# Optimization experiments

Hardware: AMD Instinct MI355X
Metric: run time of the kernel (lower is better)

## Reference

```python
import jax, jax.numpy as jnp
import numpy as np

# Dimensions: batch B, time dims P,Q, grids N, hidden nhid
B, P, Q, N, NHID = 4, 6, 4, 512, 32
WD = 4 * NHID          # wd1 = wd2 = nhid*4 = 128
AD = 2 * WD            # ad = 2*nhid*4 = 256
ALPHA = 0.2            # LeakyReLU negative slope


def setup_inputs() -> dict:
    key = jax.random.key(0)
    k1, k2, k3, k4 = jax.random.split(key, 4)
    demand = jax.random.uniform(k1, (B, P, Q, N, N), dtype=jnp.float32)
    st_feat = jax.random.normal(k2, (B, P, Q, N, WD), dtype=jnp.float32)
    # xavier_uniform with gain=1.414
    lim_W = 1.414 * np.sqrt(6.0 / (WD + WD))
    W = jax.random.uniform(k3, (WD, WD), minval=-lim_W, maxval=lim_W, dtype=jnp.float32)
    lim_a = 1.414 * np.sqrt(6.0 / (AD + 1))
    a = jax.random.uniform(k4, (AD, 1), minval=-lim_a, maxval=lim_a, dtype=jnp.float32)
    return {"demand": demand, "st_feat": st_feat, "W": W, "a": a}


def reference(demand, st_feat, W, a):
    # h = st_feat @ W : [B,P,Q,N,WD]
    h = st_feat @ W
    # GAT algebraic split: a^T [h_i || h_j] = a1.h_i + a2.h_j
    # (same math as torch repeat/cat/matmul, without the O(N^2*AD) intermediate)
    a1 = a[:WD, 0]
    a2 = a[WD:, 0]
    s1 = h @ a1  # [B,P,Q,N] -- score contribution from node i (repeated rows)
    s2 = h @ a2  # [B,P,Q,N] -- score contribution from node j (tiled rows)
    e = jax.nn.leaky_relu(s1[..., :, None] + s2[..., None, :], negative_slope=ALPHA)
    attention = jax.nn.softmax(e, axis=-1)  # softmax over j (dim=4)
    # dropout omitted: eval-mode deterministic reference
    od_matrix = jax.nn.leaky_relu(demand * attention, negative_slope=ALPHA)
    return od_matrix
```

## Files before the change

### kernel.cpp

```cpp
#include <hip/hip_runtime.h>

#define NB 4
#define NP 6
#define NQ 4
#define NN 512
#define NWD 128
#define NBPQ (NB * NP * NQ)
#define NROWS (NBPQ * NN)
#define ALPHA 0.2f

__device__ __forceinline__ float lrelu(float x) {
    return x > 0.f ? x : ALPHA * x;
}

__global__ void wa_kernel(const float* __restrict__ W, const float* __restrict__ a,
                          float* __restrict__ wa) {
    int t = threadIdx.x;
    int k = t & (NWD - 1);
    int half = t >> 7;
    const float* av = a + half * NWD;
    const float* wr = W + (long)k * NWD;
    float s = 0.f;
    #pragma unroll 8
    for (int d = 0; d < NWD; ++d) s += wr[d] * av[d];
    wa[half * NWD + k] = s;
}

__global__ __launch_bounds__(256) void s_kernel(const float* __restrict__ st,
                                                const float* __restrict__ wa,
                                                float* __restrict__ s1,
                                                float* __restrict__ s2) {
    int wid = threadIdx.x >> 6;
    int lane = threadIdx.x & 63;
    long g = (long)blockIdx.x * 4 + wid;
    const float2 f  = *reinterpret_cast<const float2*>(st + g * NWD + lane * 2);
    const float2 w1 = *reinterpret_cast<const float2*>(wa + lane * 2);
    const float2 w2 = *reinterpret_cast<const float2*>(wa + NWD + lane * 2);
    float p1 = f.x * w1.x + f.y * w1.y;
    float p2 = f.x * w2.x + f.y * w2.y;
    #pragma unroll
    for (int off = 32; off > 0; off >>= 1) {
        p1 += __shfl_xor(p1, off);
        p2 += __shfl_xor(p2, off);
    }
    if (lane == 0) { s1[g] = p1; s2[g] = p2; }
}

__global__ __launch_bounds__(256) void main_kernel(const float* __restrict__ demand,
                                                   const float* __restrict__ s1,
                                                   const float* __restrict__ s2,
                                                   float* __restrict__ out) {
    int wid = threadIdx.x >> 6;
    int lane = threadIdx.x & 63;
    long g = (long)blockIdx.x * 4 + wid;
    long slice = g >> 9;
    float s1i = s1[g];
    const float* s2s = s2 + slice * NN;

    const int c0 = lane * 4;
    const int c1 = 256 + lane * 4;
    const float4 sa = *reinterpret_cast<const float4*>(s2s + c0);
    const float4 sb = *reinterpret_cast<const float4*>(s2s + c1);

    float e[8];
    e[0] = lrelu(s1i + sa.x); e[1] = lrelu(s1i + sa.y);
    e[2] = lrelu(s1i + sa.z); e[3] = lrelu(s1i + sa.w);
    e[4] = lrelu(s1i + sb.x); e[5] = lrelu(s1i + sb.y);
    e[6] = lrelu(s1i + sb.z); e[7] = lrelu(s1i + sb.w);

    float m = e[0];
    #pragma unroll
    for (int k = 1; k < 8; ++k) m = fmaxf(m, e[k]);
    #pragma unroll
    for (int off = 32; off > 0; off >>= 1) m = fmaxf(m, __shfl_xor(m, off));

    float p[8];
    float sum = 0.f;
    #pragma unroll
    for (int k = 0; k < 8; ++k) { p[k] = expf(e[k] - m); sum += p[k]; }
    #pragma unroll
    for (int off = 32; off > 0; off >>= 1) sum += __shfl_xor(sum, off);
    const float inv = 1.f / sum;

    const float* drow = demand + g * NN;
    const float4 d0 = *reinterpret_cast<const float4*>(drow + c0);
    const float4 d1 = *reinterpret_cast<const float4*>(drow + c1);

    float4 o0, o1;
    o0.x = lrelu(d0.x * p[0] * inv); o0.y = lrelu(d0.y * p[1] * inv);
    o0.z = lrelu(d0.z * p[2] * inv); o0.w = lrelu(d0.w * p[3] * inv);
    o1.x = lrelu(d1.x * p[4] * inv); o1.y = lrelu(d1.y * p[5] * inv);
    o1.z = lrelu(d1.z * p[6] * inv); o1.w = lrelu(d1.w * p[7] * inv);

    float* orow = out + g * NN;
    *reinterpret_cast<float4*>(orow + c0) = o0;
    *reinterpret_cast<float4*>(orow + c1) = o1;
}

extern "C" void kernel_launch(void* const* d_in, const int* in_sizes, int n_in,
                              void* d_out, int out_size, void* d_ws, size_t ws_size,
                              hipStream_t stream) {
    const float* demand  = (const float*)d_in[0];
    const float* st_feat = (const float*)d_in[1];
    const float* W       = (const float*)d_in[2];
    const float* a       = (const float*)d_in[3];
    float* out = (float*)d_out;

    float* wa = (float*)d_ws;
    float* s1 = wa + 2 * NWD;
    float* s2 = s1 + NROWS;

    wa_kernel<<<1, 256, 0, stream>>>(W, a, wa);
    s_kernel<<<NROWS / 4, 256, 0, stream>>>(st_feat, wa, s1, s2);
    main_kernel<<<NROWS / 4, 256, 0, stream>>>(demand, s1, s2, out);
}
```

Measured before the change: 50.22 us.

## Fuse W·a projection into score kernel and process more rows per block

Drops the single-block wa kernel. Each block of the score kernel now recomputes W·a1 and W·a2 into shared memory, then handles 64 rows with float4 loads, two rows per wave iteration and a 32-lane reduction. This removes one launch and the serial dependency on a one-block kernel, and cuts the score kernel's grid size. The cost is that every block redundantly reads all of W, 64 KB. The softmax also switches to the fast __expf intrinsic, which is slightly less accurate.

Result: slower. 54.07 us (+7.7%).

```diff
diff --git a/kernel.cpp b/kernel.cpp
--- a/kernel.cpp
+++ b/kernel.cpp
@@ -5,45 +5,62 @@
 #define NQ 4
 #define NN 512
 #define NWD 128
-#define NBPQ (NB * NP * NQ)
-#define NROWS (NBPQ * NN)
+#define NROWS (NB * NP * NQ * NN)
 #define ALPHA 0.2f
 
 __device__ __forceinline__ float lrelu(float x) {
     return x > 0.f ? x : ALPHA * x;
 }
 
-__global__ void wa_kernel(const float* __restrict__ W, const float* __restrict__ a,
-                          float* __restrict__ wa) {
-    int t = threadIdx.x;
-    int k = t & (NWD - 1);
-    int half = t >> 7;
-    const float* av = a + half * NWD;
-    const float* wr = W + (long)k * NWD;
-    float s = 0.f;
-    #pragma unroll 8
-    for (int d = 0; d < NWD; ++d) s += wr[d] * av[d];
-    wa[half * NWD + k] = s;
-}
+__global__ __launch_bounds__(256) void s_fused_kernel(const float* __restrict__ st,
+                                                      const float* __restrict__ W,
+                                                      const float* __restrict__ a,
+                                                      float* __restrict__ s1,
+                                                      float* __restrict__ s2) {
+    __shared__ float wa1[NWD];
+    __shared__ float wa2[NWD];
 
-__global__ __launch_bounds__(256) void s_kernel(const float* __restrict__ st,
-                                                const float* __restrict__ wa,
-                                                float* __restrict__ s1,
-                                                float* __restrict__ s2) {
-    int wid = threadIdx.x >> 6;
-    int lane = threadIdx.x & 63;
-    long g = (long)blockIdx.x * 4 + wid;
-    const float2 f  = *reinterpret_cast<const float2*>(st + g * NWD + lane * 2);
-    const float2 w1 = *reinterpret_cast<const float2*>(wa + lane * 2);
-    const float2 w2 = *reinterpret_cast<const float2*>(wa + NWD + lane * 2);
-    float p1 = f.x * w1.x + f.y * w1.y;
-    float p2 = f.x * w2.x + f.y * w2.y;
+    const int t = threadIdx.x;
+    const int wid = t >> 6;
+    const int lane = t & 63;
+
+    {
+        const int k = t & (NWD - 1);
+        const float* av = a + (t >> 7) * NWD;
+        const float* wr = W + (long)k * NWD;
+        float s = 0.f;
+        #pragma unroll
+        for (int d = 0; d < NWD; d += 4) {
+            const float4 wv  = *reinterpret_cast<const float4*>(wr + d);
+            const float4 avv = *reinterpret_cast<const float4*>(av + d);
+            s += wv.x * avv.x + wv.y * avv.y + wv.z * avv.z + wv.w * avv.w;
+        }
+        if (t < NWD) wa1[k] = s; else wa2[k] = s;
+    }
+    __syncthreads();
+
+    const int l5 = lane & 31;
+    const float4 w1v = *reinterpret_cast<const float4*>(&wa1[l5 * 4]);
+    const float4 w2v = *reinterpret_cast<const float4*>(&wa2[l5 * 4]);
+    const long blockbase = (long)blockIdx.x * 64;
+
     #pragma unroll
-    for (int off = 32; off > 0; off >>= 1) {
-        p1 += __shfl_xor(p1, off);
-        p2 += __shfl_xor(p2, off);
+    for (int i = 0; i < 8; ++i) {
+        const long rowpair = blockbase + (long)wid * 16 + i * 2;
+        const float4 f = *reinterpret_cast<const float4*>(st + rowpair * NWD + lane * 4);
+        float p1 = f.x * w1v.x + f.y * w1v.y + f.z * w1v.z + f.w * w1v.w;
+        float p2 = f.x * w2v.x + f.y * w2v.y + f.z * w2v.z + f.w * w2v.w;
+        #pragma unroll
+        for (int off = 16; off > 0; off >>= 1) {
+            p1 += __shfl_xor(p1, off);
+            p2 += __shfl_xor(p2, off);
+        }
+        if (l5 == 0) {
+            const long g = rowpair + (lane >> 5);
+            s1[g] = p1;
+            s2[g] = p2;
+        }
     }
-    if (lane == 0) { s1[g] = p1; s2[g] = p2; }
 }
 
 __global__ __launch_bounds__(256) void main_kernel(const float* __restrict__ demand,
@@ -77,7 +94,7 @@
     float p[8];
     float sum = 0.f;
     #pragma unroll
-    for (int k = 0; k < 8; ++k) { p[k] = expf(e[k] - m); sum += p[k]; }
+    for (int k = 0; k < 8; ++k) { p[k] = __expf(e[k] - m); sum += p[k]; }
     #pragma unroll
     for (int off = 32; off > 0; off >>= 1) sum += __shfl_xor(sum, off);
     const float inv = 1.f / sum;
@@ -106,11 +123,9 @@
     const float* a       = (const float*)d_in[3];
     float* out = (float*)d_out;
 
-    float* wa = (float*)d_ws;
-    float* s1 = wa + 2 * NWD;
+    float* s1 = (float*)d_ws;
     float* s2 = s1 + NROWS;
 
-    wa_kernel<<<1, 256, 0, stream>>>(W, a, wa);
-    s_kernel<<<NROWS / 4, 256, 0, stream>>>(st_feat, wa, s1, s2);
+    s_fused_kernel<<<NROWS / 64, 256, 0, stream>>>(st_feat, W, a, s1, s2);
     main_kernel<<<NROWS / 4, 256, 0, stream>>>(demand, s1, s2, out);
 }
```
